# Kernel tuning notes

Hardware: AMD Instinct MI355X
Metric: run time of the kernel (lower is better)

The kernel has to match this reference:

```python
import jax, jax.numpy as jnp
import numpy as np

N_NODES = 50000
N_EDGES = 800000
HID = 128
EDGE_IN = 2 * HID + 4 + 20  # 2*hidden + edge_feat_dim + num_r_gaussian = 280


def setup_inputs() -> dict:
    key = jax.random.key(0)
    ks = jax.random.split(key, 16)
    s = lambda fan_in: 1.0 / np.sqrt(fan_in)
    inp = {
        "h": jax.random.normal(ks[0], (N_NODES, HID), dtype=jnp.float32),
        "edge_index": jax.random.randint(ks[1], (2, N_EDGES), 0, N_NODES, dtype=jnp.int64) if jax.config.jax_enable_x64 else jax.random.randint(ks[1], (2, N_EDGES), 0, N_NODES, dtype=jnp.int32),
        "edge_attr": jax.random.normal(ks[2], (N_EDGES, 24), dtype=jnp.float32),
        # edge_mlp: Linear(280->128) relu Linear(128->128) relu (act_last=True)
        "We1": jax.random.uniform(ks[3], (EDGE_IN, HID), jnp.float32, -s(EDGE_IN), s(EDGE_IN)),
        "be1": jnp.zeros((HID,), jnp.float32),
        "We2": jax.random.uniform(ks[4], (HID, HID), jnp.float32, -s(HID), s(HID)),
        "be2": jnp.zeros((HID,), jnp.float32),
        # edge_inf: Linear(128->1) + sigmoid
        "Wg": jax.random.uniform(ks[5], (HID, 1), jnp.float32, -s(HID), s(HID)),
        "bg": jnp.zeros((1,), jnp.float32),
        # node_mlp: Linear(256->128) relu Linear(128->128)
        "Wn1": jax.random.uniform(ks[6], (2 * HID, HID), jnp.float32, -s(2 * HID), s(2 * HID)),
        "bn1": jnp.zeros((HID,), jnp.float32),
        "Wn2": jax.random.uniform(ks[7], (HID, HID), jnp.float32, -s(HID), s(HID)),
        "bn2": jnp.zeros((HID,), jnp.float32),
    }
    return inp


def reference(h, edge_index, edge_attr, We1, be1, We2, be2, Wg, bg, Wn1, bn1, Wn2, bn2):
    dst, src = edge_index[0], edge_index[1]
    hi, hj = h[dst], h[src]                       # [E, HID] each
    x = jnp.concatenate([edge_attr, hi, hj], -1)  # [E, 280]
    mij = jax.nn.relu(jax.nn.relu(x @ We1 + be1) @ We2 + be2)  # [E, HID]
    eij = jax.nn.sigmoid(mij @ Wg + bg)           # [E, 1]
    mi = jax.ops.segment_sum(mij * eij, dst, num_segments=h.shape[0])  # [N, HID]
    y = jnp.concatenate([mi, h], -1)              # [N, 2*HID]
    out = jax.nn.relu(y @ Wn1 + bn1) @ Wn2 + bn2  # [N, HID]
    return out
```

## Files before the change

kernel.cpp:

```cpp
#include <hip/hip_runtime.h>

#define N_NODES 50000
#define N_EDGES 800000
#define HID 128

typedef _Float16 f16;
typedef _Float16 half8 __attribute__((ext_vector_type(8)));
typedef _Float16 half4 __attribute__((ext_vector_type(4)));
typedef _Float16 half2v __attribute__((ext_vector_type(2)));
typedef float f32x4 __attribute__((ext_vector_type(4)));
typedef float f32x2 __attribute__((ext_vector_type(2)));

#define OFF_MEDGE  0UL
#define OFF_H16C   204800000UL
#define OFF_WC     217600000UL
#define OFF_CNT    217804800UL
#define OFF_OFFS   218005504UL
#define OFF_CUR    218206208UL
#define CSR_TOTAL  218406912UL

#define OFF_MI   0UL
#define OFF_H16  25600000UL
#define OFF_W    38400000UL

#define WB1 0
#define WB2 36864
#define WN1 53248
#define WN2 86016

#define XS 296
#define TS 136
#define YS 264

#define EB 32

__global__ __launch_bounds__(256) void pack_weights(
    const float* __restrict__ We1, const float* __restrict__ We2,
    const float* __restrict__ Wn1, const float* __restrict__ Wn2,
    f16* __restrict__ W, int* __restrict__ cnt) {
  int i = blockIdx.x * 256 + threadIdx.x;
  if (cnt && i < 50176) cnt[i] = 0;
  if (i < 36864) {
    int j = i & 7, n = (i >> 3) & 127, qk = i >> 10;
    int k = qk * 8 + j;
    float v = 0.f;
    if (k < 256) v = We1[(24 + k) * 128 + n];
    else if (k < 280) v = We1[(k - 256) * 128 + n];
    W[WB1 + i] = (f16)v;
  } else if (i < 53248) {
    int l = i - 36864;
    int j = l & 7, n = (l >> 3) & 127, qk = l >> 10;
    W[WB2 + l] = (f16)We2[(qk * 8 + j) * 128 + n];
  } else if (i < 86016) {
    int l = i - 53248;
    int j = l & 7, n = (l >> 3) & 127, qk = l >> 10;
    W[WN1 + l] = (f16)Wn1[(qk * 8 + j) * 128 + n];
  } else if (i < 102400) {
    int l = i - 86016;
    int j = l & 7, n = (l >> 3) & 127, qk = l >> 10;
    W[WN2 + l] = (f16)Wn2[(qk * 8 + j) * 128 + n];
  }
}

__global__ __launch_bounds__(256) void convert_hist(
    const float* __restrict__ h, const int* __restrict__ eidx,
    f16* __restrict__ h16, int* __restrict__ cnt) {
  int i = blockIdx.x * 256 + threadIdx.x;
  const float4* src = (const float4*)h + (size_t)i * 2;
  float4 a = src[0], b = src[1];
  half8 v = {(f16)a.x, (f16)a.y, (f16)a.z, (f16)a.w,
             (f16)b.x, (f16)b.y, (f16)b.z, (f16)b.w};
  *((half8*)h16 + i) = v;
  if (cnt) atomicAdd(&cnt[eidx[i]], 1);
}

__global__ __launch_bounds__(256) void scan_kernel(const int* __restrict__ cnt,
                                                   int* __restrict__ offs, int* __restrict__ cur) {
  __shared__ int sb[256];
  int t = threadIdx.x;
  int base = t * 196;
  int s = 0;
  for (int k = 0; k < 196; ++k) s += cnt[base + k];
  sb[t] = s;
  __syncthreads();
  for (int off = 1; off < 256; off <<= 1) {
    int v = (t >= off) ? sb[t - off] : 0;
    __syncthreads();
    sb[t] += v;
    __syncthreads();
  }
  int run = sb[t] - s;
  for (int k = 0; k < 196; ++k) {
    int c = cnt[base + k];
    offs[base + k] = run;
    cur[base + k] = run;
    run += c;
  }
}

__global__ __launch_bounds__(256, 8) void edge_kernel(
    const f16* __restrict__ h16, const int* __restrict__ eidx,
    const float* __restrict__ eattr,
    const f16* __restrict__ Wp, const float* __restrict__ be1,
    const float* __restrict__ be2,
    const float* __restrict__ Wg, const float* __restrict__ bg,
    float* __restrict__ mi, f16* __restrict__ medge, int* __restrict__ cur) {
  __shared__ f16 X[EB * XS];
  __shared__ float part[EB * 4];
  __shared__ float eijL[EB];
  __shared__ int idxL[EB];
  int t = threadIdx.x;
  int e0 = blockIdx.x * EB;

  if (t < EB) {
    int d = eidx[e0 + t];
    idxL[t] = medge ? atomicAdd(&cur[d], 1) : d;
  }
  {
    int rb = t >> 4, ch = t & 15;
    for (int p = 0; p < 2; ++p) {
      int r = p * 16 + rb;
      int d = eidx[e0 + r];
      int s = eidx[N_EDGES + e0 + r];
      *(uint4*)&X[r * XS + ch * 8]       = *(const uint4*)(h16 + (size_t)d * HID + ch * 8);
      *(uint4*)&X[r * XS + 128 + ch * 8] = *(const uint4*)(h16 + (size_t)s * HID + ch * 8);
    }
  }
  if (t < 192) {
    int el = t / 6, kk = (t % 6) * 4;
    float4 f = *(const float4*)(eattr + (size_t)e0 * 24 + (size_t)t * 4);
    half4 hv = {(f16)f.x, (f16)f.y, (f16)f.z, (f16)f.w};
    *(half4*)&X[el * XS + 256 + kk] = hv;
  }
  if (t < EB) { uint4 z = {0, 0, 0, 0}; *(uint4*)&X[t * XS + 280] = z; }
  __syncthreads();

  int w = t >> 6, lane = t & 63, q = lane >> 4, c = lane & 15;
  int colBase = w * 32;
  const f16* Bp1 = Wp + WB1;
  const f16* Bp2 = Wp + WB2;

  f32x4 acc[2][2];
  {
    float b0 = be1[colBase + c], b1 = be1[colBase + 16 + c];
    #pragma unroll
    for (int mt = 0; mt < 2; ++mt) {
      acc[mt][0] = (f32x4){b0, b0, b0, b0};
      acc[mt][1] = (f32x4){b1, b1, b1, b1};
    }
  }
  const f16* bp1base = Bp1 + ((size_t)(q * 128 + colBase + c)) * 8;
  half8 bf0 = *(const half8*)(bp1base);
  half8 bf1 = *(const half8*)(bp1base + 128);
  #pragma unroll
  for (int ks = 0; ks < 9; ++ks) {
    half8 nb0, nb1;
    if (ks < 8) {
      nb0 = *(const half8*)(bp1base + (ks + 1) * 4096);
      nb1 = *(const half8*)(bp1base + (ks + 1) * 4096 + 128);
    }
    #pragma unroll
    for (int mt = 0; mt < 2; ++mt) {
      half8 a = *(const half8*)&X[(mt * 16 + c) * XS + ks * 32 + q * 8];
      acc[mt][0] = __builtin_amdgcn_mfma_f32_16x16x32_f16(a, bf0, acc[mt][0], 0, 0, 0);
      acc[mt][1] = __builtin_amdgcn_mfma_f32_16x16x32_f16(a, bf1, acc[mt][1], 0, 0, 0);
    }
    bf0 = nb0; bf1 = nb1;
  }

  const f16* bp2base = Bp2 + ((size_t)(q * 128 + colBase + c)) * 8;
  half8 d0 = *(const half8*)(bp2base);
  half8 d1 = *(const half8*)(bp2base + 128);

  __syncthreads();
  f16* T = X;
  #pragma unroll
  for (int mt = 0; mt < 2; ++mt)
    #pragma unroll
    for (int nt = 0; nt < 2; ++nt)
      #pragma unroll
      for (int r = 0; r < 4; ++r) {
        float v = acc[mt][nt][r];
        T[(mt * 16 + q * 4 + r) * TS + colBase + nt * 16 + c] = (f16)(v > 0.f ? v : 0.f);
      }
  __syncthreads();

  f32x4 m2[2][2];
  {
    float b0 = be2[colBase + c], b1 = be2[colBase + 16 + c];
    #pragma unroll
    for (int mt = 0; mt < 2; ++mt) {
      m2[mt][0] = (f32x4){b0, b0, b0, b0};
      m2[mt][1] = (f32x4){b1, b1, b1, b1};
    }
  }
  #pragma unroll
  for (int kk = 0; kk < 4; ++kk) {
    half8 n0, n1;
    if (kk < 3) {
      n0 = *(const half8*)(bp2base + (kk + 1) * 4096);
      n1 = *(const half8*)(bp2base + (kk + 1) * 4096 + 128);
    }
    #pragma unroll
    for (int mt = 0; mt < 2; ++mt) {
      half8 a = *(const half8*)&T[(mt * 16 + c) * TS + kk * 32 + q * 8];
      m2[mt][0] = __builtin_amdgcn_mfma_f32_16x16x32_f16(a, d0, m2[mt][0], 0, 0, 0);
      m2[mt][1] = __builtin_amdgcn_mfma_f32_16x16x32_f16(a, d1, m2[mt][1], 0, 0, 0);
    }
    d0 = n0; d1 = n1;
  }

  float wg0 = Wg[colBase + c], wg1 = Wg[colBase + 16 + c];
  float pd[2][4];
  #pragma unroll
  for (int mt = 0; mt < 2; ++mt)
    #pragma unroll
    for (int r = 0; r < 4; ++r) {
      float v0 = m2[mt][0][r]; v0 = v0 > 0.f ? v0 : 0.f; m2[mt][0][r] = v0;
      float v1 = m2[mt][1][r]; v1 = v1 > 0.f ? v1 : 0.f; m2[mt][1][r] = v1;
      pd[mt][r] = v0 * wg0 + v1 * wg1;
    }
  #pragma unroll
  for (int off = 1; off < 16; off <<= 1)
    #pragma unroll
    for (int mt = 0; mt < 2; ++mt)
      #pragma unroll
      for (int r = 0; r < 4; ++r)
        pd[mt][r] += __shfl_xor(pd[mt][r], off, 64);
  if (c == 0)
    #pragma unroll
    for (int mt = 0; mt < 2; ++mt)
      #pragma unroll
      for (int r = 0; r < 4; ++r)
        part[(mt * 16 + q * 4 + r) * 4 + w] = pd[mt][r];
  __syncthreads();
  if (t < EB) {
    float s = part[t * 4] + part[t * 4 + 1] + part[t * 4 + 2] + part[t * 4 + 3] + bg[0];
    eijL[t] = 1.f / (1.f + __expf(-s));
  }
  __syncthreads();

  if (medge) {
    #pragma unroll
    for (int mt = 0; mt < 2; ++mt)
      #pragma unroll
      for (int r = 0; r < 4; ++r) {
        int el = mt * 16 + q * 4 + r;
        float ev = eijL[el];
        T[el * TS + colBase + c]      = (f16)(m2[mt][0][r] * ev);
        T[el * TS + colBase + 16 + c] = (f16)(m2[mt][1][r] * ev);
      }
    __syncthreads();
    int r = t >> 3, p = t & 7;
    uint4* dst = (uint4*)(medge + (size_t)idxL[r] * HID + p * 16);
    const uint4* s = (const uint4*)&T[r * TS + p * 16];
    dst[0] = s[0]; dst[1] = s[1];
  } else {
    #pragma unroll
    for (int mt = 0; mt < 2; ++mt)
      #pragma unroll
      for (int r = 0; r < 4; ++r) {
        int el = mt * 16 + q * 4 + r;
        float ev = eijL[el];
        float* base = mi + (size_t)idxL[el] * HID + colBase + c;
        atomicAdd(base,      m2[mt][0][r] * ev);
        atomicAdd(base + 16, m2[mt][1][r] * ev);
      }
  }
}

__global__ __launch_bounds__(256) void segsum_kernel(
    const f16* __restrict__ medge, const int* __restrict__ offs,
    const int* __restrict__ cnt, float* __restrict__ mi) {
  int t = threadIdx.x;
  int g = blockIdx.x * 4 + (t >> 6);
  int l = t & 63;
  int start = offs[g], deg = cnt[g];
  const f16* base = medge + (size_t)start * HID + 2 * l;
  float ax = 0.f, ay = 0.f;
  #pragma unroll 4
  for (int i = 0; i < deg; ++i) {
    half2v v = *(const half2v*)(base + (size_t)i * HID);
    ax += (float)v[0]; ay += (float)v[1];
  }
  f32x2 o = {ax, ay};
  *(f32x2*)(mi + (size_t)g * HID + 2 * l) = o;
}

__global__ __launch_bounds__(256, 4) void node_kernel(
    const float* mi, const f16* __restrict__ h16,
    const f16* __restrict__ Wp, const float* __restrict__ bn1,
    const float* __restrict__ bn2, float* out) {
  __shared__ f16 Y[64 * YS];
  int t = threadIdx.x;
  int n0 = blockIdx.x * 64;
  {
    int rb = t >> 4, ch = t & 15;
    for (int p = 0; p < 4; ++p) {
      int r = p * 16 + rb;
      int g = n0 + r; if (g >= N_NODES) g = N_NODES - 1;
      const float4* s = (const float4*)(mi + (size_t)g * HID + ch * 8);
      float4 a = s[0], b = s[1];
      half8 v = {(f16)a.x, (f16)a.y, (f16)a.z, (f16)a.w,
                 (f16)b.x, (f16)b.y, (f16)b.z, (f16)b.w};
      *(half8*)&Y[r * YS + ch * 8] = v;
      *(uint4*)&Y[r * YS + 128 + ch * 8] = *(const uint4*)(h16 + (size_t)g * HID + ch * 8);
    }
  }
  __syncthreads();
  int w = t >> 6, lane = t & 63, q = lane >> 4, c = lane & 15;
  int colBase = w * 32;
  const f16* BN1 = Wp + WN1;
  const f16* BN2 = Wp + WN2;
  f32x4 acc[4][2];
  {
    float b0 = bn1[colBase + c], b1 = bn1[colBase + 16 + c];
    #pragma unroll
    for (int mt = 0; mt < 4; ++mt) {
      acc[mt][0] = (f32x4){b0, b0, b0, b0};
      acc[mt][1] = (f32x4){b1, b1, b1, b1};
    }
  }
  const f16* bn1base = BN1 + ((size_t)(q * 128 + colBase + c)) * 8;
  half8 bf0 = *(const half8*)(bn1base);
  half8 bf1 = *(const half8*)(bn1base + 128);
  #pragma unroll
  for (int ks = 0; ks < 8; ++ks) {
    half8 nb0, nb1;
    if (ks < 7) {
      nb0 = *(const half8*)(bn1base + (ks + 1) * 4096);
      nb1 = *(const half8*)(bn1base + (ks + 1) * 4096 + 128);
    }
    #pragma unroll
    for (int mt = 0; mt < 4; ++mt) {
      half8 a = *(const half8*)&Y[(mt * 16 + c) * YS + ks * 32 + q * 8];
      acc[mt][0] = __builtin_amdgcn_mfma_f32_16x16x32_f16(a, bf0, acc[mt][0], 0, 0, 0);
      acc[mt][1] = __builtin_amdgcn_mfma_f32_16x16x32_f16(a, bf1, acc[mt][1], 0, 0, 0);
    }
    bf0 = nb0; bf1 = nb1;
  }
  const f16* bn2base = BN2 + ((size_t)(q * 128 + colBase + c)) * 8;
  half8 d0 = *(const half8*)(bn2base);
  half8 d1 = *(const half8*)(bn2base + 128);
  __syncthreads();
  f16* T = Y;
  #pragma unroll
  for (int mt = 0; mt < 4; ++mt)
    #pragma unroll
    for (int nt = 0; nt < 2; ++nt)
      #pragma unroll
      for (int r = 0; r < 4; ++r) {
        float v = acc[mt][nt][r];
        T[(mt * 16 + q * 4 + r) * TS + colBase + nt * 16 + c] = (f16)(v > 0.f ? v : 0.f);
      }
  __syncthreads();
  f32x4 m2[4][2];
  {
    float b0 = bn2[colBase + c], b1 = bn2[colBase + 16 + c];
    #pragma unroll
    for (int mt = 0; mt < 4; ++mt) {
      m2[mt][0] = (f32x4){b0, b0, b0, b0};
      m2[mt][1] = (f32x4){b1, b1, b1, b1};
    }
  }
  #pragma unroll
  for (int kk = 0; kk < 4; ++kk) {
    half8 n0, n1;
    if (kk < 3) {
      n0 = *(const half8*)(bn2base + (kk + 1) * 4096);
      n1 = *(const half8*)(bn2base + (kk + 1) * 4096 + 128);
    }
    #pragma unroll
    for (int mt = 0; mt < 4; ++mt) {
      half8 a = *(const half8*)&T[(mt * 16 + c) * TS + kk * 32 + q * 8];
      m2[mt][0] = __builtin_amdgcn_mfma_f32_16x16x32_f16(a, d0, m2[mt][0], 0, 0, 0);
      m2[mt][1] = __builtin_amdgcn_mfma_f32_16x16x32_f16(a, d1, m2[mt][1], 0, 0, 0);
    }
    d0 = n0; d1 = n1;
  }
  #pragma unroll
  for (int mt = 0; mt < 4; ++mt)
    #pragma unroll
    for (int r = 0; r < 4; ++r) {
      int g = n0 + mt * 16 + q * 4 + r;
      if (g < N_NODES) {
        float* o = out + (size_t)g * HID + colBase + c;
        o[0]  = m2[mt][0][r];
        o[16] = m2[mt][1][r];
      }
    }
}

extern "C" void kernel_launch(void* const* d_in, const int* in_sizes, int n_in,
                              void* d_out, int out_size, void* d_ws, size_t ws_size,
                              hipStream_t stream) {
  const float* h    = (const float*)d_in[0];
  const int*   eidx = (const int*)d_in[1];
  const float* eattr= (const float*)d_in[2];
  const float* We1  = (const float*)d_in[3];
  const float* be1  = (const float*)d_in[4];
  const float* We2  = (const float*)d_in[5];
  const float* be2  = (const float*)d_in[6];
  const float* Wg   = (const float*)d_in[7];
  const float* bg   = (const float*)d_in[8];
  const float* Wn1  = (const float*)d_in[9];
  const float* bn1  = (const float*)d_in[10];
  const float* Wn2  = (const float*)d_in[11];
  const float* bn2  = (const float*)d_in[12];
  float* out = (float*)d_out;
  char* ws = (char*)d_ws;

  if (ws_size >= CSR_TOTAL) {
    f16* medge = (f16*)(ws + OFF_MEDGE);
    f16* h16   = (f16*)(ws + OFF_H16C);
    f16* Wp    = (f16*)(ws + OFF_WC);
    int* cnt   = (int*)(ws + OFF_CNT);
    int* offs  = (int*)(ws + OFF_OFFS);
    int* cur   = (int*)(ws + OFF_CUR);
    float* mi  = out;

    pack_weights<<<400, 256, 0, stream>>>(We1, We2, Wn1, Wn2, Wp, cnt);
    convert_hist<<<3125, 256, 0, stream>>>(h, eidx, h16, cnt);
    scan_kernel<<<1, 256, 0, stream>>>(cnt, offs, cur);
    edge_kernel<<<N_EDGES / EB, 256, 0, stream>>>(h16, eidx, eattr, Wp, be1, be2,
                                                  Wg, bg, nullptr, medge, cur);
    segsum_kernel<<<N_NODES / 4, 256, 0, stream>>>(medge, offs, cnt, mi);
    node_kernel<<<(N_NODES + 63) / 64, 256, 0, stream>>>(mi, h16, Wp, bn1, bn2, out);
  } else {
    float* mi  = (float*)(ws + OFF_MI);
    f16*   h16 = (f16*)(ws + OFF_H16);
    f16*   Wp  = (f16*)(ws + OFF_W);

    hipMemsetAsync(mi, 0, (size_t)N_NODES * HID * sizeof(float), stream);
    pack_weights<<<400, 256, 0, stream>>>(We1, We2, Wn1, Wn2, Wp, nullptr);
    convert_hist<<<3125, 256, 0, stream>>>(h, eidx, h16, nullptr);
    edge_kernel<<<N_EDGES / EB, 256, 0, stream>>>(h16, eidx, eattr, Wp, be1, be2,
                                                  Wg, bg, mi, nullptr, nullptr);
    node_kernel<<<(N_NODES + 63) / 64, 256, 0, stream>>>(mi, h16, Wp, bn1, bn2, out);
  }
}
```

Before: 464.0 us.

## Precompute per-node first-layer projections and gather them per edge

Splits the first edge-MLP layer algebraically: h@W_dst and h@W_src are computed once per node into a buffer stored in the output array, and each edge gathers and adds the two projected rows instead of running the 256-wide K loop. Only the 24-wide edge-attribute part remains as an MFMA per edge. The CSR path also builds an explicit dst-sorted permutation, so edges are processed in sorted order and medge is written contiguously instead of scattered through atomics. The cost is an extra precompute kernel, wider per-edge gathers of projected rows, and fp16 rounding of the partial sums.

```diff
diff --git a/kernel.cpp b/kernel.cpp
--- a/kernel.cpp
+++ b/kernel.cpp
@@ -17,7 +17,8 @@
 #define OFF_CNT    217804800UL
 #define OFF_OFFS   218005504UL
 #define OFF_CUR    218206208UL
-#define CSR_TOTAL  218406912UL
+#define OFF_PERM   218406912UL
+#define CSR_TOTAL  221606912UL
 
 #define OFF_MI   0UL
 #define OFF_H16  25600000UL
@@ -28,9 +29,10 @@
 #define WN1 53248
 #define WN2 86016
 
-#define XS 296
 #define TS 136
 #define YS 264
+#define SS 132
+#define AS 40
 
 #define EB 32
 
@@ -98,47 +100,112 @@
   }
 }
 
+__global__ __launch_bounds__(256) void fill_perm(
+    const int* __restrict__ eidx, int* __restrict__ cur, int* __restrict__ perm) {
+  int i = blockIdx.x * 256 + threadIdx.x;
+  int p = atomicAdd(&cur[eidx[i]], 1);
+  perm[p] = i;
+}
+
+__global__ __launch_bounds__(256, 4) void precompute_kernel(
+    const f16* __restrict__ h16, const f16* __restrict__ Wp, f16* __restrict__ P) {
+  __shared__ f16 Y[64 * 136];
+  int t = threadIdx.x;
+  int n0 = blockIdx.x * 64;
+  {
+    int rb = t >> 4, ch = t & 15;
+    for (int p = 0; p < 4; ++p) {
+      int r = p * 16 + rb;
+      int g = n0 + r; if (g >= N_NODES) g = N_NODES - 1;
+      *(uint4*)&Y[r * 136 + ch * 8] = *(const uint4*)(h16 + (size_t)g * HID + ch * 8);
+    }
+  }
+  __syncthreads();
+  int w = t >> 6, lane = t & 63, q = lane >> 4, c = lane & 15;
+  int colBase = w * 32;
+  const f16* B = Wp + WB1 + ((size_t)(q * 128 + colBase + c)) * 8;
+  f32x4 aD[4][2], aS[4][2];
+  #pragma unroll
+  for (int mt = 0; mt < 4; ++mt) {
+    aD[mt][0] = (f32x4){0, 0, 0, 0}; aD[mt][1] = (f32x4){0, 0, 0, 0};
+    aS[mt][0] = (f32x4){0, 0, 0, 0}; aS[mt][1] = (f32x4){0, 0, 0, 0};
+  }
+  #pragma unroll
+  for (int ks = 0; ks < 4; ++ks) {
+    half8 bD0 = *(const half8*)(B + ks * 4096);
+    half8 bD1 = *(const half8*)(B + ks * 4096 + 128);
+    half8 bS0 = *(const half8*)(B + (ks + 4) * 4096);
+    half8 bS1 = *(const half8*)(B + (ks + 4) * 4096 + 128);
+    #pragma unroll
+    for (int mt = 0; mt < 4; ++mt) {
+      half8 a = *(const half8*)&Y[(mt * 16 + c) * 136 + ks * 32 + q * 8];
+      aD[mt][0] = __builtin_amdgcn_mfma_f32_16x16x32_f16(a, bD0, aD[mt][0], 0, 0, 0);
+      aD[mt][1] = __builtin_amdgcn_mfma_f32_16x16x32_f16(a, bD1, aD[mt][1], 0, 0, 0);
+      aS[mt][0] = __builtin_amdgcn_mfma_f32_16x16x32_f16(a, bS0, aS[mt][0], 0, 0, 0);
+      aS[mt][1] = __builtin_amdgcn_mfma_f32_16x16x32_f16(a, bS1, aS[mt][1], 0, 0, 0);
+    }
+  }
+  #pragma unroll
+  for (int mt = 0; mt < 4; ++mt)
+    #pragma unroll
+    for (int r = 0; r < 4; ++r) {
+      int g = n0 + mt * 16 + q * 4 + r;
+      if (g < N_NODES) {
+        f16* o = P + (size_t)g * 256 + colBase + c;
+        o[0]        = (f16)aD[mt][0][r];
+        o[16]       = (f16)aD[mt][1][r];
+        o[128]      = (f16)aS[mt][0][r];
+        o[128 + 16] = (f16)aS[mt][1][r];
+      }
+    }
+}
+
 __global__ __launch_bounds__(256, 8) void edge_kernel(
-    const f16* __restrict__ h16, const int* __restrict__ eidx,
+    const f16* __restrict__ P, const int* __restrict__ eidx,
     const float* __restrict__ eattr,
     const f16* __restrict__ Wp, const float* __restrict__ be1,
     const float* __restrict__ be2,
     const float* __restrict__ Wg, const float* __restrict__ bg,
-    float* __restrict__ mi, f16* __restrict__ medge, int* __restrict__ cur) {
-  __shared__ f16 X[EB * XS];
+    float* __restrict__ mi, f16* __restrict__ medge, const int* __restrict__ perm) {
+  __shared__ float S[EB * SS];
+  __shared__ f16 A[EB * AS];
   __shared__ float part[EB * 4];
   __shared__ float eijL[EB];
-  __shared__ int idxL[EB];
+  __shared__ int dstL[EB];
   int t = threadIdx.x;
   int e0 = blockIdx.x * EB;
 
-  if (t < EB) {
-    int d = eidx[e0 + t];
-    idxL[t] = medge ? atomicAdd(&cur[d], 1) : d;
-  }
+  if (!medge && t < EB) dstL[t] = eidx[e0 + t];
+
   {
     int rb = t >> 4, ch = t & 15;
     for (int p = 0; p < 2; ++p) {
       int r = p * 16 + rb;
-      int d = eidx[e0 + r];
-      int s = eidx[N_EDGES + e0 + r];
-      *(uint4*)&X[r * XS + ch * 8]       = *(const uint4*)(h16 + (size_t)d * HID + ch * 8);
-      *(uint4*)&X[r * XS + 128 + ch * 8] = *(const uint4*)(h16 + (size_t)s * HID + ch * 8);
+      int e = perm ? perm[e0 + r] : (e0 + r);
+      int d = eidx[e];
+      int s = eidx[N_EDGES + e];
+      half8 pd = *(const half8*)(P + (size_t)d * 256 + ch * 8);
+      half8 ps = *(const half8*)(P + (size_t)s * 256 + 128 + ch * 8);
+      f32x4 lo = {(float)pd[0] + (float)ps[0], (float)pd[1] + (float)ps[1],
+                  (float)pd[2] + (float)ps[2], (float)pd[3] + (float)ps[3]};
+      f32x4 hi = {(float)pd[4] + (float)ps[4], (float)pd[5] + (float)ps[5],
+                  (float)pd[6] + (float)ps[6], (float)pd[7] + (float)ps[7]};
+      *(f32x4*)&S[r * SS + ch * 8]     = lo;
+      *(f32x4*)&S[r * SS + ch * 8 + 4] = hi;
     }
   }
   if (t < 192) {
-    int el = t / 6, kk = (t % 6) * 4;
-    float4 f = *(const float4*)(eattr + (size_t)e0 * 24 + (size_t)t * 4);
+    int el = t / 6, kk = t % 6;
+    int e = perm ? perm[e0 + el] : (e0 + el);
+    float4 f = *(const float4*)(eattr + (size_t)e * 24 + kk * 4);
     half4 hv = {(f16)f.x, (f16)f.y, (f16)f.z, (f16)f.w};
-    *(half4*)&X[el * XS + 256 + kk] = hv;
-  }
-  if (t < EB) { uint4 z = {0, 0, 0, 0}; *(uint4*)&X[t * XS + 280] = z; }
+    *(half4*)&A[el * AS + kk * 4] = hv;
+  }
+  if (t < EB) { uint4 z = {0, 0, 0, 0}; *(uint4*)&A[t * AS + 24] = z; }
   __syncthreads();
 
   int w = t >> 6, lane = t & 63, q = lane >> 4, c = lane & 15;
   int colBase = w * 32;
-  const f16* Bp1 = Wp + WB1;
-  const f16* Bp2 = Wp + WB2;
 
   f32x4 acc[2][2];
   {
@@ -149,31 +216,32 @@
       acc[mt][1] = (f32x4){b1, b1, b1, b1};
     }
   }
-  const f16* bp1base = Bp1 + ((size_t)(q * 128 + colBase + c)) * 8;
-  half8 bf0 = *(const half8*)(bp1base);
-  half8 bf1 = *(const half8*)(bp1base + 128);
-  #pragma unroll
-  for (int ks = 0; ks < 9; ++ks) {
-    half8 nb0, nb1;
-    if (ks < 8) {
-      nb0 = *(const half8*)(bp1base + (ks + 1) * 4096);
-      nb1 = *(const half8*)(bp1base + (ks + 1) * 4096 + 128);
-    }
+  {
+    const f16* bA = Wp + WB1 + 32768 + ((size_t)(q * 128 + colBase + c)) * 8;
+    half8 b0f = *(const half8*)(bA);
+    half8 b1f = *(const half8*)(bA + 128);
     #pragma unroll
     for (int mt = 0; mt < 2; ++mt) {
-      half8 a = *(const half8*)&X[(mt * 16 + c) * XS + ks * 32 + q * 8];
-      acc[mt][0] = __builtin_amdgcn_mfma_f32_16x16x32_f16(a, bf0, acc[mt][0], 0, 0, 0);
-      acc[mt][1] = __builtin_amdgcn_mfma_f32_16x16x32_f16(a, bf1, acc[mt][1], 0, 0, 0);
-    }
-    bf0 = nb0; bf1 = nb1;
-  }
-
-  const f16* bp2base = Bp2 + ((size_t)(q * 128 + colBase + c)) * 8;
+      half8 a = *(const half8*)&A[(mt * 16 + c) * AS + q * 8];
+      acc[mt][0] = __builtin_amdgcn_mfma_f32_16x16x32_f16(a, b0f, acc[mt][0], 0, 0, 0);
+      acc[mt][1] = __builtin_amdgcn_mfma_f32_16x16x32_f16(a, b1f, acc[mt][1], 0, 0, 0);
+    }
+  }
+  #pragma unroll
+  for (int mt = 0; mt < 2; ++mt)
+    #pragma unroll
+    for (int r = 0; r < 4; ++r) {
+      const float* sr = &S[(mt * 16 + q * 4 + r) * SS + colBase + c];
+      acc[mt][0][r] += sr[0];
+      acc[mt][1][r] += sr[16];
+    }
+
+  const f16* bp2base = Wp + WB2 + ((size_t)(q * 128 + colBase + c)) * 8;
   half8 d0 = *(const half8*)(bp2base);
   half8 d1 = *(const half8*)(bp2base + 128);
 
   __syncthreads();
-  f16* T = X;
+  f16* T = (f16*)S;
   #pragma unroll
   for (int mt = 0; mt < 2; ++mt)
     #pragma unroll
@@ -252,9 +320,9 @@
       }
     __syncthreads();
     int r = t >> 3, p = t & 7;
-    uint4* dst = (uint4*)(medge + (size_t)idxL[r] * HID + p * 16);
-    const uint4* s = (const uint4*)&T[r * TS + p * 16];
-    dst[0] = s[0]; dst[1] = s[1];
+    uint4* dst = (uint4*)(medge + ((size_t)(e0 + r)) * HID + p * 16);
+    const uint4* s2 = (const uint4*)&T[r * TS + p * 16];
+    dst[0] = s2[0]; dst[1] = s2[1];
   } else {
     #pragma unroll
     for (int mt = 0; mt < 2; ++mt)
@@ -262,7 +330,7 @@
       for (int r = 0; r < 4; ++r) {
         int el = mt * 16 + q * 4 + r;
         float ev = eijL[el];
-        float* base = mi + (size_t)idxL[el] * HID + colBase + c;
+        float* base = mi + (size_t)dstL[el] * HID + colBase + c;
         atomicAdd(base,      m2[mt][0][r] * ev);
         atomicAdd(base + 16, m2[mt][1][r] * ev);
       }
@@ -417,24 +485,30 @@
     int* cnt   = (int*)(ws + OFF_CNT);
     int* offs  = (int*)(ws + OFF_OFFS);
     int* cur   = (int*)(ws + OFF_CUR);
+    int* perm  = (int*)(ws + OFF_PERM);
+    f16* P     = (f16*)out;
     float* mi  = out;
 
     pack_weights<<<400, 256, 0, stream>>>(We1, We2, Wn1, Wn2, Wp, cnt);
     convert_hist<<<3125, 256, 0, stream>>>(h, eidx, h16, cnt);
     scan_kernel<<<1, 256, 0, stream>>>(cnt, offs, cur);
-    edge_kernel<<<N_EDGES / EB, 256, 0, stream>>>(h16, eidx, eattr, Wp, be1, be2,
-                                                  Wg, bg, nullptr, medge, cur);
+    precompute_kernel<<<(N_NODES + 63) / 64, 256, 0, stream>>>(h16, Wp, P);
+    fill_perm<<<3125, 256, 0, stream>>>(eidx, cur, perm);
+    edge_kernel<<<N_EDGES / EB, 256, 0, stream>>>(P, eidx, eattr, Wp, be1, be2,
+                                                  Wg, bg, nullptr, medge, perm);
     segsum_kernel<<<N_NODES / 4, 256, 0, stream>>>(medge, offs, cnt, mi);
     node_kernel<<<(N_NODES + 63) / 64, 256, 0, stream>>>(mi, h16, Wp, bn1, bn2, out);
   } else {
     float* mi  = (float*)(ws + OFF_MI);
     f16*   h16 = (f16*)(ws + OFF_H16);
     f16*   Wp  = (f16*)(ws + OFF_W);
+    f16*   P   = (f16*)out;
 
     hipMemsetAsync(mi, 0, (size_t)N_NODES * HID * sizeof(float), stream);
     pack_weights<<<400, 256, 0, stream>>>(We1, We2, Wn1, Wn2, Wp, nullptr);
     convert_hist<<<3125, 256, 0, stream>>>(h, eidx, h16, nullptr);
-    edge_kernel<<<N_EDGES / EB, 256, 0, stream>>>(h16, eidx, eattr, Wp, be1, be2,
+    precompute_kernel<<<(N_NODES + 63) / 64, 256, 0, stream>>>(h16, Wp, P);
+    edge_kernel<<<N_EDGES / EB, 256, 0, stream>>>(P, eidx, eattr, Wp, be1, be2,
                                                   Wg, bg, mi, nullptr, nullptr);
     node_kernel<<<(N_NODES + 63) / 64, 256, 0, stream>>>(mi, h16, Wp, bn1, bn2, out);
   }
```

After: 496.6 us. 7.0% more time.
